# Optimization experiments

Measured on AMD Instinct MI355X. Metric: run time of the kernel, lower is better.

## Reference

```python
import jax, jax.numpy as jnp
import numpy as np

N_NODES = 50000
N_EDGES = 800000
IN_DIM = 128
HIDDEN = 16
HEADS1 = 8
OUT_DIM = 128
NEG_SLOPE = 0.2
EPS = 1e-16


def gat_conv(x, src, dst, W, att_src, att_dst, bias, heads, out_ch, concat, num_nodes):
    # x: [N, F_in]; W: [F_in, heads*out_ch]; att_*: [heads, out_ch]; bias: [heads*out_ch] or [out_ch]
    h = (x @ W).reshape(num_nodes, heads, out_ch)          # [N, H, C]
    a_src = jnp.einsum('nhc,hc->nh', h, att_src)           # [N, H]
    a_dst = jnp.einsum('nhc,hc->nh', h, att_dst)           # [N, H]
    alpha = a_src[src] + a_dst[dst]                        # [E, H]
    alpha = jax.nn.leaky_relu(alpha, NEG_SLOPE)
    # segment softmax over incoming edges of each dst node
    amax = jax.ops.segment_max(alpha, dst, num_segments=num_nodes)  # [N, H]
    e = jnp.exp(alpha - amax[dst])                         # [E, H]
    denom = jax.ops.segment_sum(e, dst, num_segments=num_nodes)     # [N, H]
    alpha = e / (denom[dst] + EPS)                         # [E, H]
    msg = h[src] * alpha[:, :, None]                       # [E, H, C]
    out = jax.ops.segment_sum(msg, dst, num_segments=num_nodes)     # [N, H, C]
    if concat:
        out = out.reshape(num_nodes, heads * out_ch)
    else:
        out = out.mean(axis=1)
    return out + bias


def setup_inputs() -> dict:
    key = jax.random.key(0)
    ks = jax.random.split(key, 12)
    x = jax.random.normal(ks[0], (N_NODES, IN_DIM), dtype=jnp.float32)
    edge_index = jax.random.randint(ks[1], (2, N_EDGES), 0, N_NODES, dtype=jnp.int32)
    s1 = 1.0 / np.sqrt(IN_DIM)
    s2 = 1.0 / np.sqrt(HIDDEN * HEADS1)
    W1 = jax.random.normal(ks[2], (IN_DIM, HEADS1 * HIDDEN), dtype=jnp.float32) * s1
    att_src1 = jax.random.normal(ks[3], (HEADS1, HIDDEN), dtype=jnp.float32) * s1
    att_dst1 = jax.random.normal(ks[4], (HEADS1, HIDDEN), dtype=jnp.float32) * s1
    bias1 = jnp.zeros((HEADS1 * HIDDEN,), dtype=jnp.float32)
    W2 = jax.random.normal(ks[5], (HEADS1 * HIDDEN, OUT_DIM), dtype=jnp.float32) * s2
    att_src2 = jax.random.normal(ks[6], (1, OUT_DIM), dtype=jnp.float32) * s2
    att_dst2 = jax.random.normal(ks[7], (1, OUT_DIM), dtype=jnp.float32) * s2
    bias2 = jnp.zeros((OUT_DIM,), dtype=jnp.float32)
    return {"x": x, "edge_index": edge_index,
            "W1": W1, "att_src1": att_src1, "att_dst1": att_dst1, "bias1": bias1,
            "W2": W2, "att_src2": att_src2, "att_dst2": att_dst2, "bias2": bias2}


def reference(x, edge_index, W1, att_src1, att_dst1, bias1, W2, att_src2, att_dst2, bias2):
    # eval mode: F.dropout and attention dropout are identity
    src, dst = edge_index[0], edge_index[1]
    h = gat_conv(x, src, dst, W1, att_src1, att_dst1, bias1,
                 HEADS1, HIDDEN, True, N_NODES)            # [N, HEADS1*HIDDEN]
    h = jax.nn.elu(h)
    out = gat_conv(h, src, dst, W2, att_src2, att_dst2, bias2,
                   1, OUT_DIM, False, N_NODES)             # [N, OUT_DIM]
    return out
```

## Files before the change

### kernel.cpp

```cpp
#include <hip/hip_runtime.h>

#define N_NODES 50000
#define N_EDGES 800000
#define CAP 64
#define NBUCK 196
#define NODES_PAD 50176
#define BBLK 256
#define EPB 3125

typedef unsigned int uint;
typedef unsigned short ushort;
typedef __attribute__((ext_vector_type(4))) float f32x4;
typedef __attribute__((ext_vector_type(8))) short s16x8;

__device__ __forceinline__ ushort f2bf(float f) {
    uint u = __float_as_uint(f);
    u = (u + 0x7fffu + ((u >> 16) & 1u)) >> 16;
    return (ushort)u;
}
__device__ __forceinline__ float bf_lo(uint u) { return __uint_as_float(u << 16); }
__device__ __forceinline__ float bf_hi(uint u) { return __uint_as_float(u & 0xffff0000u); }

__global__ __launch_bounds__(256) void bin_count_kernel(
    const int* __restrict__ dstv, uint* __restrict__ counts)
{
    __shared__ uint hist[NBUCK];
    int tid = threadIdx.x, b = blockIdx.x;
    for (int k = tid; k < NBUCK; k += 256) hist[k] = 0;
    __syncthreads();
    int e0 = b * EPB;
    for (int i = tid; i < EPB; i += 256)
        atomicAdd(&hist[((uint)dstv[e0 + i]) >> 8], 1u);
    __syncthreads();
    for (int k = tid; k < NBUCK; k += 256) counts[k * BBLK + b] = hist[k];
}

__global__ __launch_bounds__(256) void scan_kernel(
    const uint* __restrict__ counts, uint* __restrict__ ofs)
{
    __shared__ uint wsum[4];
    int tid = threadIdx.x;
    int lane = tid & 63, wid = tid >> 6;
    int base = tid * NBUCK;
    uint s = 0;
    for (int i = 0; i < NBUCK; i++) s += counts[base + i];
    uint inc = s;
    #pragma unroll
    for (int o = 1; o < 64; o <<= 1) {
        uint v = __shfl_up(inc, o);
        if (lane >= o) inc += v;
    }
    if (lane == 63) wsum[wid] = inc;
    __syncthreads();
    uint wo = 0;
    for (int w = 0; w < wid; w++) wo += wsum[w];
    uint off = wo + inc - s;
    for (int i = 0; i < NBUCK; i++) {
        uint v = counts[base + i];
        ofs[base + i] = off;
        off += v;
    }
    if (tid == 255) ofs[NODES_PAD] = off;
}

__global__ __launch_bounds__(256) void bin_scatter_kernel(
    const int* __restrict__ srcv, const int* __restrict__ dstv,
    const uint* __restrict__ ofs, uint* __restrict__ binned)
{
    __shared__ uint cur[NBUCK];
    int tid = threadIdx.x, b = blockIdx.x;
    for (int k = tid; k < NBUCK; k += 256) cur[k] = ofs[k * BBLK + b];
    __syncthreads();
    int e0 = b * EPB;
    for (int i = tid; i < EPB; i += 256) {
        int d = dstv[e0 + i], s = srcv[e0 + i];
        uint k = ((uint)d) >> 8;
        uint pos = atomicAdd(&cur[k], 1u);
        binned[pos] = (((uint)d & 255u) << 16) | (uint)s;
    }
}

__global__ __launch_bounds__(256) void build_kernel(
    const uint* __restrict__ binned, const uint* __restrict__ ofs,
    int* __restrict__ deg, int* __restrict__ list)
{
    __shared__ uint ldeg[256];
    __shared__ uint llist[256 * CAP];
    int tid = threadIdx.x, k = blockIdx.x;
    ldeg[tid] = 0;
    __syncthreads();
    uint start = ofs[k * BBLK];
    uint end = ofs[(k + 1) * BBLK];
    for (uint i = start + tid; i < end; i += 256) {
        uint p = binned[i];
        uint nl = (p >> 16) & 255u;
        uint slot = atomicAdd(&ldeg[nl], 1u);
        if (slot < CAP) llist[(nl << 6) + slot] = p & 0xFFFFu;
    }
    __syncthreads();
    int node0 = k << 8;
    deg[node0 + tid] = (int)ldeg[tid];
    uint4* d4 = (uint4*)(list + (size_t)node0 * CAP);
    const uint4* s4 = (const uint4*)llist;
    for (int i = tid; i < 256 * CAP / 4; i += 256) d4[i] = s4[i];
}

__global__ __launch_bounds__(256) void prep_kernel(
    const float* __restrict__ W1, const float* __restrict__ as1, const float* __restrict__ ad1,
    const float* __restrict__ W2, const float* __restrict__ as2, const float* __restrict__ ad2,
    float* __restrict__ WS1, float* __restrict__ WS2)
{
    int idx = blockIdx.x * 256 + threadIdx.x;
    if (idx < 2048) {
        int k = idx >> 4, j = idx & 15;
        const float* att = (j < 8) ? as1 : ad1;
        int head = j & 7;
        float s = 0.f;
        #pragma unroll
        for (int c = 0; c < 16; c++)
            s += W1[k * 128 + head * 16 + c] * att[head * 16 + c];
        WS1[idx] = s;
    } else if (idx < 4096) {
        int idx2 = idx - 2048;
        int k = idx2 >> 4, j = idx2 & 15;
        float s = 0.f;
        if (j < 2) {
            const float* att = j ? ad2 : as2;
            for (int c = 0; c < 128; c++) s += W2[k * 128 + c] * att[c];
        }
        WS2[idx2] = s;
    }
}

template <int HEADS, bool ABF16>
__global__ __launch_bounds__(512) void gemm_mfma_kernel(
    const void* __restrict__ Av, const float* __restrict__ W,
    const float* __restrict__ WS,
    ushort* __restrict__ h16, float* __restrict__ a_src, float* __restrict__ a_dst,
    int nrows)
{
    __shared__ ushort Bf[2304 * 8];
    int tid = threadIdx.x;
    for (int idx = tid; idx < 2304; idx += 512) {
        int t = idx >> 8;
        int rem = idx & 255;
        int kt = rem >> 6, L = rem & 63;
        int col = L & 15;
        int kb = ((L >> 4) << 3) + (kt << 5);
        ushort tmp[8];
        if (t < 8) {
            #pragma unroll
            for (int j = 0; j < 8; j++)
                tmp[j] = f2bf(W[(size_t)(kb + j) * 128 + (t << 4) + col]);
        } else {
            #pragma unroll
            for (int j = 0; j < 8; j++)
                tmp[j] = f2bf(WS[(kb + j) * 16 + col]);
        }
        uint p0 = (uint)tmp[0] | ((uint)tmp[1] << 16);
        uint p1 = (uint)tmp[2] | ((uint)tmp[3] << 16);
        uint p2 = (uint)tmp[4] | ((uint)tmp[5] << 16);
        uint p3 = (uint)tmp[6] | ((uint)tmp[7] << 16);
        *(uint4*)&Bf[idx * 8] = make_uint4(p0, p1, p2, p3);
    }
    __syncthreads();

    int lane = tid & 63;
    int wv = tid >> 6;
    int row0 = (blockIdx.x * 8 + wv) * 16;
    if (row0 >= nrows) return;

    int m = lane & 15, kg = lane >> 4;
    s16x8 afrag[4];
    if (ABF16) {
        const ushort* arow = (const ushort*)Av + (size_t)(row0 + m) * 128 + (kg << 3);
        #pragma unroll
        for (int kt = 0; kt < 4; kt++)
            afrag[kt] = *(const s16x8*)(arow + (kt << 5));
    } else {
        const float* arow = (const float*)Av + (size_t)(row0 + m) * 128 + (kg << 3);
        #pragma unroll
        for (int kt = 0; kt < 4; kt++) {
            float4 f0 = *(const float4*)(arow + (kt << 5));
            float4 f1 = *(const float4*)(arow + (kt << 5) + 4);
            union { s16x8 v; ushort us[8]; } uu;
            uu.us[0] = f2bf(f0.x); uu.us[1] = f2bf(f0.y);
            uu.us[2] = f2bf(f0.z); uu.us[3] = f2bf(f0.w);
            uu.us[4] = f2bf(f1.x); uu.us[5] = f2bf(f1.y);
            uu.us[6] = f2bf(f1.z); uu.us[7] = f2bf(f1.w);
            afrag[kt] = uu.v;
        }
    }

    f32x4 acc[9];
    #pragma unroll
    for (int t = 0; t < 9; t++) acc[t] = (f32x4){0.f, 0.f, 0.f, 0.f};
    #pragma unroll
    for (int t = 0; t < 9; t++) {
        #pragma unroll
        for (int kt = 0; kt < 4; kt++) {
            s16x8 b = *(const s16x8*)&Bf[(((t << 2) + kt) * 64 + lane) * 8];
            acc[t] = __builtin_amdgcn_mfma_f32_16x16x32_bf16(afrag[kt], b, acc[t], 0, 0, 0);
        }
    }

    int colw = lane & 15;
    int rbase = row0 + ((lane >> 4) << 2);
    #pragma unroll
    for (int t = 0; t < 8; t++) {
        #pragma unroll
        for (int r = 0; r < 4; r++)
            h16[(size_t)(rbase + r) * 128 + (t << 4) + colw] = f2bf(acc[t][r]);
    }
    #pragma unroll
    for (int r = 0; r < 4; r++) {
        float v = acc[8][r];
        int row = rbase + r;
        if (HEADS == 8) {
            if (colw < 8) a_src[row * 8 + colw] = v;
            else          a_dst[row * 8 + (colw - 8)] = v;
        } else {
            if (colw == 0)      a_src[row] = v;
            else if (colw == 1) a_dst[row] = v;
        }
    }
}

template <int HEADS, bool ELU, bool OUT16>
__global__ __launch_bounds__(256) void agg_kernel(
    const ushort* __restrict__ h16, const int* __restrict__ list, const int* __restrict__ deg,
    const float* __restrict__ a_src, const float* __restrict__ a_dst,
    const float* __restrict__ bias, void* __restrict__ outv)
{
    __shared__ float w_lds[4][HEADS][65];
    __shared__ int s_lds[4][64];
    int lane = threadIdx.x & 63;
    int wv = threadIdx.x >> 6;
    int n = blockIdx.x * 4 + wv;
    int d = min(deg[n], CAP);
    bool valid = lane < d;
    int s = valid ? list[n * CAP + lane] : 0;
    s_lds[wv][lane] = s;

    float eh[HEADS], sh[HEADS];
    if (HEADS == 8) {
        float4 u0 = *(const float4*)&a_src[s * 8];
        float4 u1 = *(const float4*)&a_src[s * 8 + 4];
        float4 v0 = *(const float4*)&a_dst[n * 8];
        float4 v1 = *(const float4*)&a_dst[n * 8 + 4];
        float al[8] = {u0.x + v0.x, u0.y + v0.y, u0.z + v0.z, u0.w + v0.w,
                       u1.x + v1.x, u1.y + v1.y, u1.z + v1.z, u1.w + v1.w};
        #pragma unroll
        for (int hh = 0; hh < 8; hh++) {
            float a = al[hh];
            a = a > 0.f ? a : 0.2f * a;
            eh[hh] = valid ? __expf(a) : 0.f;
            sh[hh] = eh[hh];
        }
    } else {
        float a = a_src[s] + a_dst[n];
        a = a > 0.f ? a : 0.2f * a;
        eh[0] = valid ? __expf(a) : 0.f;
        sh[0] = eh[0];
    }
    #pragma unroll
    for (int mm = 1; mm < 16; mm <<= 1) {
        #pragma unroll
        for (int hh = 0; hh < HEADS; hh++) sh[hh] += __shfl_xor(sh[hh], mm);
    }
    if (d > 16) {
        #pragma unroll
        for (int hh = 0; hh < HEADS; hh++) sh[hh] += __shfl_xor(sh[hh], 16);
    }
    if (d > 32) {
        #pragma unroll
        for (int hh = 0; hh < HEADS; hh++) sh[hh] += __shfl_xor(sh[hh], 32);
    }
    #pragma unroll
    for (int hh = 0; hh < HEADS; hh++)
        w_lds[wv][hh][lane] = eh[hh] / (sh[hh] + 1e-16f);
    __syncthreads();

    int c0 = lane << 1;
    int g = (HEADS == 8) ? (lane >> 3) : 0;
    const ushort* hbase = h16 + c0;
    float acc0 = 0.f, acc1 = 0.f;
    int d16 = (d + 15) & ~15;
    for (int e0 = 0; e0 < d16; e0 += 16) {
        uint u[16]; float w[16];
        #pragma unroll
        for (int j = 0; j < 16; j++) {
            int ss = s_lds[wv][e0 + j];
            u[j] = *(const uint*)(hbase + (size_t)ss * 128);
            w[j] = w_lds[wv][g][e0 + j];
        }
        #pragma unroll
        for (int j = 0; j < 16; j++) {
            acc0 = fmaf(w[j], bf_lo(u[j]), acc0);
            acc1 = fmaf(w[j], bf_hi(u[j]), acc1);
        }
    }
    float o0 = acc0 + bias[c0];
    float o1 = acc1 + bias[c0 + 1];
    if (ELU) {
        o0 = o0 > 0.f ? o0 : __expf(o0) - 1.f;
        o1 = o1 > 0.f ? o1 : __expf(o1) - 1.f;
    }
    if (OUT16) {
        uint pk = (uint)f2bf(o0) | ((uint)f2bf(o1) << 16);
        *(uint*)((ushort*)outv + (size_t)n * 128 + c0) = pk;
    } else {
        *(float2*)((float*)outv + (size_t)n * 128 + c0) = make_float2(o0, o1);
    }
}

extern "C" void kernel_launch(void* const* d_in, const int* in_sizes, int n_in,
                              void* d_out, int out_size, void* d_ws, size_t ws_size,
                              hipStream_t stream)
{
    (void)in_sizes; (void)n_in; (void)out_size; (void)ws_size;
    const float* x   = (const float*)d_in[0];
    const int*   ei  = (const int*)d_in[1];
    const float* W1  = (const float*)d_in[2];
    const float* as1 = (const float*)d_in[3];
    const float* ad1 = (const float*)d_in[4];
    const float* b1  = (const float*)d_in[5];
    const float* W2  = (const float*)d_in[6];
    const float* as2 = (const float*)d_in[7];
    const float* ad2 = (const float*)d_in[8];
    const float* b2  = (const float*)d_in[9];
    float* out = (float*)d_out;
    const int* srcv = ei;
    const int* dstv = ei + N_EDGES;

    char* ws = (char*)d_ws;
    size_t off = 0;
    auto alloc = [&](size_t bytes) {
        void* p = ws + off;
        off += (bytes + 255) & ~(size_t)255;
        return p;
    };
    ushort* h1_16 = (ushort*)alloc((size_t)N_NODES * 128 * 2);
    ushort* h2_16 = (ushort*)alloc((size_t)N_NODES * 128 * 2);
    ushort* h1b   = (ushort*)alloc((size_t)N_NODES * 128 * 2);
    float*  asrc1 = (float*)alloc((size_t)N_NODES * 8 * 4);
    float*  adst1 = (float*)alloc((size_t)N_NODES * 8 * 4);
    float*  asrc2 = (float*)alloc((size_t)N_NODES * 4);
    float*  adst2 = (float*)alloc((size_t)N_NODES * 4);
    int*    degp  = (int*)alloc((size_t)NODES_PAD * 4);
    int*    list  = (int*)alloc((size_t)NODES_PAD * CAP * 4);
    float*  WS1   = (float*)alloc(128 * 16 * 4);
    float*  WS2   = (float*)alloc(128 * 16 * 4);
    uint* binned = (uint*)h1b;
    uint* counts = binned + N_EDGES;
    uint* ofsp   = counts + NODES_PAD;

    const int NG = (N_NODES + 3) / 4;
    const int GB = (N_NODES / 16 + 7) / 8;

    prep_kernel<<<16, 256, 0, stream>>>(W1, as1, ad1, W2, as2, ad2, WS1, WS2);
    bin_count_kernel<<<BBLK, 256, 0, stream>>>(dstv, counts);
    scan_kernel<<<1, 256, 0, stream>>>(counts, ofsp);
    bin_scatter_kernel<<<BBLK, 256, 0, stream>>>(srcv, dstv, ofsp, binned);
    build_kernel<<<NBUCK, 256, 0, stream>>>(binned, ofsp, degp, list);

    gemm_mfma_kernel<8, false><<<GB, 512, 0, stream>>>(x, W1, WS1, h1_16, asrc1, adst1, N_NODES);
    agg_kernel<8, true, true><<<NG, 256, 0, stream>>>(h1_16, list, degp, asrc1, adst1, b1, h1b);

    gemm_mfma_kernel<1, true><<<GB, 512, 0, stream>>>(h1b, W2, WS2, h2_16, asrc2, adst2, N_NODES);
    agg_kernel<1, false, false><<<NG, 256, 0, stream>>>(h2_16, list, degp, asrc2, adst2, b2, out);
}
```

Baseline: 145.7 us.

## Parallelize offset scan, shrink adjacency to u16, restructure aggregation with packed math

```diff
diff --git a/kernel.cpp b/kernel.cpp
--- a/kernel.cpp
+++ b/kernel.cpp
@@ -7,11 +7,29 @@
 #define NODES_PAD 50176
 #define BBLK 256
 #define EPB 3125
+#define LOG2E 1.4426950408889634f
 
 typedef unsigned int uint;
 typedef unsigned short ushort;
+typedef __attribute__((ext_vector_type(2))) float f32x2;
 typedef __attribute__((ext_vector_type(4))) float f32x4;
 typedef __attribute__((ext_vector_type(8))) short s16x8;
+
+__device__ __forceinline__ f32x2 pk_add(f32x2 a, f32x2 b) {
+    f32x2 d;
+    asm("v_pk_add_f32 %0, %1, %2" : "=v"(d) : "v"(a), "v"(b));
+    return d;
+}
+__device__ __forceinline__ f32x2 pk_mul(f32x2 a, f32x2 b) {
+    f32x2 d;
+    asm("v_pk_mul_f32 %0, %1, %2" : "=v"(d) : "v"(a), "v"(b));
+    return d;
+}
+__device__ __forceinline__ f32x2 pk_fma(f32x2 a, f32x2 b, f32x2 c) {
+    f32x2 d;
+    asm("v_pk_fma_f32 %0, %1, %2, %3" : "=v"(d) : "v"(a), "v"(b), "v"(c));
+    return d;
+}
 
 __device__ __forceinline__ ushort f2bf(float f) {
     uint u = __float_as_uint(f);
@@ -35,41 +53,58 @@
     for (int k = tid; k < NBUCK; k += 256) counts[k * BBLK + b] = hist[k];
 }
 
-__global__ __launch_bounds__(256) void scan_kernel(
-    const uint* __restrict__ counts, uint* __restrict__ ofs)
-{
-    __shared__ uint wsum[4];
-    int tid = threadIdx.x;
+__global__ __launch_bounds__(256) void scan1_kernel(
+    const uint* __restrict__ counts, uint* __restrict__ ofs, uint* __restrict__ bsum)
+{
+    __shared__ uint wtot[4];
+    int tid = threadIdx.x, k = blockIdx.x;
     int lane = tid & 63, wid = tid >> 6;
-    int base = tid * NBUCK;
-    uint s = 0;
-    for (int i = 0; i < NBUCK; i++) s += counts[base + i];
+    uint v = counts[k * 256 + tid];
+    uint inc = v;
+    #pragma unroll
+    for (int o = 1; o < 64; o <<= 1) {
+        uint t = __shfl_up(inc, o);
+        if (lane >= o) inc += t;
+    }
+    if (lane == 63) wtot[wid] = inc;
+    __syncthreads();
+    uint woff = 0;
+    for (int w = 0; w < wid; w++) woff += wtot[w];
+    uint excl = woff + inc - v;
+    ofs[k * 256 + tid] = excl;
+    if (tid == 255) bsum[k] = excl + v;
+}
+
+__global__ __launch_bounds__(64) void scan2_kernel(
+    const uint* __restrict__ bsum, uint* __restrict__ bbase)
+{
+    int lane = threadIdx.x;
+    int base = lane * 4;
+    uint v[4];
+    #pragma unroll
+    for (int j = 0; j < 4; j++) v[j] = (base + j < NBUCK) ? bsum[base + j] : 0u;
+    uint s = v[0] + v[1] + v[2] + v[3];
     uint inc = s;
     #pragma unroll
     for (int o = 1; o < 64; o <<= 1) {
-        uint v = __shfl_up(inc, o);
-        if (lane >= o) inc += v;
-    }
-    if (lane == 63) wsum[wid] = inc;
-    __syncthreads();
-    uint wo = 0;
-    for (int w = 0; w < wid; w++) wo += wsum[w];
-    uint off = wo + inc - s;
-    for (int i = 0; i < NBUCK; i++) {
-        uint v = counts[base + i];
-        ofs[base + i] = off;
-        off += v;
-    }
-    if (tid == 255) ofs[NODES_PAD] = off;
+        uint t = __shfl_up(inc, o);
+        if (lane >= o) inc += t;
+    }
+    uint run = inc - s;
+    #pragma unroll
+    for (int j = 0; j < 4; j++) {
+        if (base + j < NBUCK) { bbase[base + j] = run; run += v[j]; }
+    }
 }
 
 __global__ __launch_bounds__(256) void bin_scatter_kernel(
     const int* __restrict__ srcv, const int* __restrict__ dstv,
-    const uint* __restrict__ ofs, uint* __restrict__ binned)
+    const uint* __restrict__ ofs, const uint* __restrict__ bbase,
+    uint* __restrict__ binned)
 {
     __shared__ uint cur[NBUCK];
     int tid = threadIdx.x, b = blockIdx.x;
-    for (int k = tid; k < NBUCK; k += 256) cur[k] = ofs[k * BBLK + b];
+    for (int k = tid; k < NBUCK; k += 256) cur[k] = ofs[k * BBLK + b] + bbase[k];
     __syncthreads();
     int e0 = b * EPB;
     for (int i = tid; i < EPB; i += 256) {
@@ -82,27 +117,28 @@
 
 __global__ __launch_bounds__(256) void build_kernel(
     const uint* __restrict__ binned, const uint* __restrict__ ofs,
-    int* __restrict__ deg, int* __restrict__ list)
+    const uint* __restrict__ bbase,
+    int* __restrict__ deg, ushort* __restrict__ list)
 {
     __shared__ uint ldeg[256];
-    __shared__ uint llist[256 * CAP];
+    __shared__ ushort llist[256 * CAP];
     int tid = threadIdx.x, k = blockIdx.x;
     ldeg[tid] = 0;
     __syncthreads();
-    uint start = ofs[k * BBLK];
-    uint end = ofs[(k + 1) * BBLK];
+    uint start = ofs[k * 256] + bbase[k];
+    uint end = (k == NBUCK - 1) ? N_EDGES : (ofs[(k + 1) * 256] + bbase[k + 1]);
     for (uint i = start + tid; i < end; i += 256) {
         uint p = binned[i];
         uint nl = (p >> 16) & 255u;
         uint slot = atomicAdd(&ldeg[nl], 1u);
-        if (slot < CAP) llist[(nl << 6) + slot] = p & 0xFFFFu;
+        if (slot < CAP) llist[(nl << 6) + slot] = (ushort)(p & 0xFFFFu);
     }
     __syncthreads();
     int node0 = k << 8;
     deg[node0 + tid] = (int)ldeg[tid];
     uint4* d4 = (uint4*)(list + (size_t)node0 * CAP);
     const uint4* s4 = (const uint4*)llist;
-    for (int i = tid; i < 256 * CAP / 4; i += 256) d4[i] = s4[i];
+    for (int i = tid; i < 256 * CAP * 2 / 16; i += 256) d4[i] = s4[i];
 }
 
 __global__ __launch_bounds__(256) void prep_kernel(
@@ -119,7 +155,7 @@
         #pragma unroll
         for (int c = 0; c < 16; c++)
             s += W1[k * 128 + head * 16 + c] * att[head * 16 + c];
-        WS1[idx] = s;
+        WS1[idx] = s * LOG2E;
     } else if (idx < 4096) {
         int idx2 = idx - 2048;
         int k = idx2 >> 4, j = idx2 & 15;
@@ -128,7 +164,7 @@
             const float* att = j ? ad2 : as2;
             for (int c = 0; c < 128; c++) s += W2[k * 128 + c] * att[c];
         }
-        WS2[idx2] = s;
+        WS2[idx2] = s * LOG2E;
     }
 }
 
@@ -228,21 +264,22 @@
 
 template <int HEADS, bool ELU, bool OUT16>
 __global__ __launch_bounds__(256) void agg_kernel(
-    const ushort* __restrict__ h16, const int* __restrict__ list, const int* __restrict__ deg,
+    const ushort* __restrict__ h16, const ushort* __restrict__ list,
+    const int* __restrict__ deg,
     const float* __restrict__ a_src, const float* __restrict__ a_dst,
     const float* __restrict__ bias, void* __restrict__ outv)
 {
     __shared__ float w_lds[4][HEADS][65];
     __shared__ int s_lds[4][64];
+    __shared__ float sh_l[4][8];
     int lane = threadIdx.x & 63;
     int wv = threadIdx.x >> 6;
     int n = blockIdx.x * 4 + wv;
     int d = min(deg[n], CAP);
     bool valid = lane < d;
-    int s = valid ? list[n * CAP + lane] : 0;
-    s_lds[wv][lane] = s;
-
-    float eh[HEADS], sh[HEADS];
+    int s = valid ? (int)list[n * CAP + lane] : 0;
+    s_lds[wv][lane] = s << 8;
+
     if (HEADS == 8) {
         float4 u0 = *(const float4*)&a_src[s * 8];
         float4 u1 = *(const float4*)&a_src[s * 8 + 4];
@@ -250,67 +287,96 @@
         float4 v1 = *(const float4*)&a_dst[n * 8 + 4];
         float al[8] = {u0.x + v0.x, u0.y + v0.y, u0.z + v0.z, u0.w + v0.w,
                        u1.x + v1.x, u1.y + v1.y, u1.z + v1.z, u1.w + v1.w};
+        float eh[8];
         #pragma unroll
         for (int hh = 0; hh < 8; hh++) {
-            float a = al[hh];
-            a = a > 0.f ? a : 0.2f * a;
-            eh[hh] = valid ? __expf(a) : 0.f;
-            sh[hh] = eh[hh];
+            float a = fmaxf(al[hh], 0.2f * al[hh]);
+            eh[hh] = valid ? exp2f(a) : 0.f;
+            w_lds[wv][hh][lane] = eh[hh];
+        }
+        f32x2 s01 = {eh[0], eh[1]}, s23 = {eh[2], eh[3]};
+        f32x2 s45 = {eh[4], eh[5]}, s67 = {eh[6], eh[7]};
+        auto lvl = [&](int mm) {
+            f32x2 t;
+            t.x = __shfl_xor(s01.x, mm); t.y = __shfl_xor(s01.y, mm); s01 = pk_add(s01, t);
+            t.x = __shfl_xor(s23.x, mm); t.y = __shfl_xor(s23.y, mm); s23 = pk_add(s23, t);
+            t.x = __shfl_xor(s45.x, mm); t.y = __shfl_xor(s45.y, mm); s45 = pk_add(s45, t);
+            t.x = __shfl_xor(s67.x, mm); t.y = __shfl_xor(s67.y, mm); s67 = pk_add(s67, t);
+        };
+        lvl(1); lvl(2); lvl(4); lvl(8);
+        if (d > 16) lvl(16);
+        if (d > 32) lvl(32);
+        if (lane == 0) {
+            *(f32x2*)&sh_l[wv][0] = s01; *(f32x2*)&sh_l[wv][2] = s23;
+            *(f32x2*)&sh_l[wv][4] = s45; *(f32x2*)&sh_l[wv][6] = s67;
         }
     } else {
         float a = a_src[s] + a_dst[n];
-        a = a > 0.f ? a : 0.2f * a;
-        eh[0] = valid ? __expf(a) : 0.f;
-        sh[0] = eh[0];
-    }
-    #pragma unroll
-    for (int mm = 1; mm < 16; mm <<= 1) {
-        #pragma unroll
-        for (int hh = 0; hh < HEADS; hh++) sh[hh] += __shfl_xor(sh[hh], mm);
-    }
-    if (d > 16) {
-        #pragma unroll
-        for (int hh = 0; hh < HEADS; hh++) sh[hh] += __shfl_xor(sh[hh], 16);
-    }
-    if (d > 32) {
-        #pragma unroll
-        for (int hh = 0; hh < HEADS; hh++) sh[hh] += __shfl_xor(sh[hh], 32);
-    }
-    #pragma unroll
-    for (int hh = 0; hh < HEADS; hh++)
-        w_lds[wv][hh][lane] = eh[hh] / (sh[hh] + 1e-16f);
-    __syncthreads();
-
-    int c0 = lane << 1;
-    int g = (HEADS == 8) ? (lane >> 3) : 0;
-    const ushort* hbase = h16 + c0;
-    float acc0 = 0.f, acc1 = 0.f;
-    int d16 = (d + 15) & ~15;
-    for (int e0 = 0; e0 < d16; e0 += 16) {
-        uint u[16]; float w[16];
-        #pragma unroll
-        for (int j = 0; j < 16; j++) {
-            int ss = s_lds[wv][e0 + j];
-            u[j] = *(const uint*)(hbase + (size_t)ss * 128);
-            w[j] = w_lds[wv][g][e0 + j];
-        }
-        #pragma unroll
-        for (int j = 0; j < 16; j++) {
-            acc0 = fmaf(w[j], bf_lo(u[j]), acc0);
-            acc1 = fmaf(w[j], bf_hi(u[j]), acc1);
-        }
-    }
-    float o0 = acc0 + bias[c0];
-    float o1 = acc1 + bias[c0 + 1];
+        a = fmaxf(a, 0.2f * a);
+        float eh0 = valid ? exp2f(a) : 0.f;
+        w_lds[wv][0][lane] = eh0;
+        float sh = eh0;
+        sh += __shfl_xor(sh, 1); sh += __shfl_xor(sh, 2);
+        sh += __shfl_xor(sh, 4); sh += __shfl_xor(sh, 8);
+        if (d > 16) sh += __shfl_xor(sh, 16);
+        if (d > 32) sh += __shfl_xor(sh, 32);
+        if (lane == 0) sh_l[wv][0] = sh;
+    }
+
+    int half = lane >> 5;
+    int lq = lane & 31;
+    int c0 = lq << 2;
+    int g = (HEADS == 8) ? (lq >> 2) : 0;
+    const char* hp = (const char*)h16 + (c0 << 1);
+    f32x2 acc01 = {0.f, 0.f}, acc23 = {0.f, 0.f};
+    int d8 = (d + 7) & ~7;
+    for (int e0 = 0; e0 < d8; e0 += 8) {
+        int soff[4]; float wv4[4]; uint2 u[4];
+        #pragma unroll
+        for (int r = 0; r < 4; r++) {
+            int e = e0 + (r << 1) + half;
+            soff[r] = s_lds[wv][e];
+            wv4[r] = w_lds[wv][g][e];
+        }
+        #pragma unroll
+        for (int r = 0; r < 4; r++)
+            u[r] = *(const uint2*)(hp + soff[r]);
+        #pragma unroll
+        for (int r = 0; r < 4; r++) {
+            f32x2 wp = {wv4[r], wv4[r]};
+            f32x2 lo = {bf_lo(u[r].x), bf_hi(u[r].x)};
+            f32x2 hi = {bf_lo(u[r].y), bf_hi(u[r].y)};
+            acc01 = pk_fma(wp, lo, acc01);
+            acc23 = pk_fma(wp, hi, acc23);
+        }
+    }
+    f32x2 t;
+    t.x = __shfl_xor(acc01.x, 32); t.y = __shfl_xor(acc01.y, 32); acc01 = pk_add(acc01, t);
+    t.x = __shfl_xor(acc23.x, 32); t.y = __shfl_xor(acc23.y, 32); acc23 = pk_add(acc23, t);
+
+    float shv = sh_l[wv][g];
+    float r = __builtin_amdgcn_rcpf(shv + 1e-16f);
+    f32x2 rr = {r, r};
+    acc01 = pk_mul(acc01, rr);
+    acc23 = pk_mul(acc23, rr);
+    float4 bv = *(const float4*)&bias[c0];
+    float o0 = acc01.x + bv.x, o1 = acc01.y + bv.y;
+    float o2 = acc23.x + bv.z, o3 = acc23.y + bv.w;
     if (ELU) {
         o0 = o0 > 0.f ? o0 : __expf(o0) - 1.f;
         o1 = o1 > 0.f ? o1 : __expf(o1) - 1.f;
-    }
-    if (OUT16) {
-        uint pk = (uint)f2bf(o0) | ((uint)f2bf(o1) << 16);
-        *(uint*)((ushort*)outv + (size_t)n * 128 + c0) = pk;
-    } else {
-        *(float2*)((float*)outv + (size_t)n * 128 + c0) = make_float2(o0, o1);
+        o2 = o2 > 0.f ? o2 : __expf(o2) - 1.f;
+        o3 = o3 > 0.f ? o3 : __expf(o3) - 1.f;
+    }
+    if (lane < 32) {
+        if (OUT16) {
+            uint2 pk;
+            pk.x = (uint)f2bf(o0) | ((uint)f2bf(o1) << 16);
+            pk.y = (uint)f2bf(o2) | ((uint)f2bf(o3) << 16);
+            *(uint2*)((ushort*)outv + (size_t)n * 128 + c0) = pk;
+        } else {
+            *(float4*)((float*)outv + (size_t)n * 128 + c0) = make_float4(o0, o1, o2, o3);
+        }
     }
 }
 
@@ -348,21 +414,24 @@
     float*  asrc2 = (float*)alloc((size_t)N_NODES * 4);
     float*  adst2 = (float*)alloc((size_t)N_NODES * 4);
     int*    degp  = (int*)alloc((size_t)NODES_PAD * 4);
-    int*    list  = (int*)alloc((size_t)NODES_PAD * CAP * 4);
+    ushort* list  = (ushort*)alloc((size_t)NODES_PAD * CAP * 2);
     float*  WS1   = (float*)alloc(128 * 16 * 4);
     float*  WS2   = (float*)alloc(128 * 16 * 4);
     uint* binned = (uint*)h1b;
     uint* counts = binned + N_EDGES;
     uint* ofsp   = counts + NODES_PAD;
+    uint* bsum   = ofsp + NODES_PAD;
+    uint* bbase  = bsum + NBUCK;
 
     const int NG = (N_NODES + 3) / 4;
     const int GB = (N_NODES / 16 + 7) / 8;
 
     prep_kernel<<<16, 256, 0, stream>>>(W1, as1, ad1, W2, as2, ad2, WS1, WS2);
     bin_count_kernel<<<BBLK, 256, 0, stream>>>(dstv, counts);
-    scan_kernel<<<1, 256, 0, stream>>>(counts, ofsp);
-    bin_scatter_kernel<<<BBLK, 256, 0, stream>>>(srcv, dstv, ofsp, binned);
-    build_kernel<<<NBUCK, 256, 0, stream>>>(binned, ofsp, degp, list);
+    scan1_kernel<<<NBUCK, 256, 0, stream>>>(counts, ofsp, bsum);
+    scan2_kernel<<<1, 64, 0, stream>>>(bsum, bbase);
+    bin_scatter_kernel<<<BBLK, 256, 0, stream>>>(srcv, dstv, ofsp, bbase, binned);
+    build_kernel<<<NBUCK, 256, 0, stream>>>(binned, ofsp, bbase, degp, list);
 
     gemm_mfma_kernel<8, false><<<GB, 512, 0, stream>>>(x, W1, WS1, h1_16, asrc1, adst1, N_NODES);
     agg_kernel<8, true, true><<<NG, 256, 0, stream>>>(h1_16, list, degp, asrc1, adst1, b1, h1b);
```

Measured after the change: 125.5 us. 13.9% less time.
